# Optimization experiments

Measured on AMD Instinct MI355X. Metric: run time of the kernel, lower is better.

Reference implementation:

```python
import jax, jax.numpy as jnp
import numpy as np

N = 100_000   # nodes
E = 3_200_000 # edges
G = 128       # graphs in batch
H = 32        # hidden_dim
PI = float(np.pi)


def setup_inputs() -> dict:
    key = jax.random.key(0)
    ks = jax.random.split(key, 18)
    p = lambda k, s: (jax.random.normal(k, s, dtype=jnp.float32) * 0.1)
    x = jax.random.normal(ks[0], (N, 1), dtype=jnp.float32)
    edge_index = jax.random.randint(ks[1], (2, E), 0, N, dtype=jnp.int32)
    batch = jnp.sort(jax.random.randint(ks[2], (N,), 0, G, dtype=jnp.int32))
    return dict(
        x=x, edge_index=edge_index, batch=batch,
        W1=p(ks[3], (1, H)),  b1=jnp.zeros((H,), jnp.float32),
        W2=p(ks[4], (H, H)),  b2=jnp.zeros((H,), jnp.float32),
        W3=p(ks[5], (H, H)),  b3=jnp.zeros((H,), jnp.float32),
        Wt1=p(ks[6], (H, 32)), bt1=jnp.zeros((32,), jnp.float32),
        Wt2=p(ks[7], (32, 1)), bt2=jnp.zeros((1,), jnp.float32),
        Wg1=p(ks[8], (H, 32)), bg1=jnp.zeros((32,), jnp.float32),
        Wg2=p(ks[9], (32, 2)), bg2=jnp.zeros((2,), jnp.float32),
    )


def _gcn_norm(edge_index):
    # PyG GCNConv default: add self-loops, symmetric normalization.
    loop = jnp.arange(N, dtype=edge_index.dtype)
    src = jnp.concatenate([edge_index[0], loop])
    dst = jnp.concatenate([edge_index[1], loop])
    deg = jax.ops.segment_sum(jnp.ones_like(dst, dtype=jnp.float32), dst, num_segments=N)
    dinv = jnp.where(deg > 0, jax.lax.rsqrt(jnp.maximum(deg, 1.0)), 0.0)
    norm = dinv[src] * dinv[dst]  # [E+N]
    return src, dst, norm


def _gcn_conv(x, W, b, src, dst, norm):
    h = x @ W                                  # [N, out]
    msg = h[src] * norm[:, None]               # gather + scale  [E+N, out]
    return jax.ops.segment_sum(msg, dst, num_segments=N) + b


def _forward(x, W1, b1, W2, b2, W3, b3, Wt1, bt1, Wt2, bt2, Wg1, bg1, Wg2, bg2,
             edge_index, batch):
    src, dst, norm = _gcn_norm(edge_index)
    x = jax.nn.relu(_gcn_conv(x, W1, b1, src, dst, norm))
    x = jax.nn.relu(_gcn_conv(x, W2, b2, src, dst, norm))
    h = jax.nn.relu(_gcn_conv(x, W3, b3, src, dst, norm))
    # theta head per node
    theta = PI * jax.nn.sigmoid(jax.nn.relu(h @ Wt1 + bt1) @ Wt2 + bt2)[:, 0]  # [N]
    # global mean pool per graph
    counts = jax.ops.segment_sum(jnp.ones((N,), jnp.float32), batch, num_segments=G)
    gsum = jax.ops.segment_sum(h, batch, num_segments=G)
    gemb = gsum / jnp.maximum(counts, 1.0)[:, None]                            # [G, H]
    beta_gamma = 2.0 * PI * jax.nn.sigmoid(jax.nn.relu(gemb @ Wg1 + bg1) @ Wg2 + bg2)  # [G, 2]
    return theta, beta_gamma


def reference(x, edge_index, batch, W1, b1, W2, b2, W3, b3,
              Wt1, bt1, Wt2, bt2, Wg1, bg1, Wg2, bg2):
    return _forward(x, W1, b1, W2, b2, W3, b3, Wt1, bt1, Wt2, bt2,
                    Wg1, bg1, Wg2, bg2, edge_index, batch)
```

## Files before the change

kernel.cpp:

```cpp
#include <hip/hip_runtime.h>
#include <hip/hip_bf16.h>

#define PI_F 3.14159265358979323846f
#define NBLK 256
#define BSH 8
#define BSZ 256
#define SCAP 10240
#define SLDS 3072

static inline size_t align256(size_t x) { return (x + 255) & ~size_t(255); }

typedef float v2f __attribute__((ext_vector_type(2)));
typedef unsigned uvec4 __attribute__((ext_vector_type(4)));

__device__ __forceinline__ unsigned bfpack(float a, float b) {
    unsigned lo = (__float_as_uint(a) + 0x8000u) >> 16;
    unsigned hi = (__float_as_uint(b) + 0x8000u) & 0xFFFF0000u;
    return lo | hi;
}

__device__ __forceinline__ void f8acc(uint2 q, float rs, float acc[8]) {
    v2f l0 = __builtin_amdgcn_cvt_pk_f32_fp8(q.x, false);
    v2f h0 = __builtin_amdgcn_cvt_pk_f32_fp8(q.x, true);
    v2f l1 = __builtin_amdgcn_cvt_pk_f32_fp8(q.y, false);
    v2f h1 = __builtin_amdgcn_cvt_pk_f32_fp8(q.y, true);
    acc[0] += rs * l0.x; acc[1] += rs * l0.y; acc[2] += rs * h0.x; acc[3] += rs * h0.y;
    acc[4] += rs * l1.x; acc[5] += rs * l1.y; acc[6] += rs * h1.x; acc[7] += rs * h1.y;
}


__global__ void __launch_bounds__(1024) count_kernel(
                             const int* __restrict__ dst, int* __restrict__ C,
                             int E, int CHUNK, int NB2) {
    extern __shared__ int hist[];
    for (int i = threadIdx.x; i < NB2; i += 1024) hist[i] = 0;
    __syncthreads();
    int s0 = blockIdx.x * CHUNK, s1 = min(s0 + CHUNK, E);
    for (int e = s0 + threadIdx.x; e < s1; e += 1024)
        atomicAdd(&hist[dst[e] >> BSH], 1);
    __syncthreads();
    for (int i = threadIdx.x; i < NB2; i += 1024)
        C[(size_t)blockIdx.x * NB2 + i] = hist[i];
}

__global__ void scan_blocks_kernel(int* __restrict__ C, int* __restrict__ colsum, int NB2) {
    __shared__ int s[256];
    int k = blockIdx.x;
    int b = threadIdx.x;
    int v = C[(size_t)b * NB2 + k];
    s[b] = v;
    __syncthreads();
    for (int off = 1; off < 256; off <<= 1) {
        int w = (b >= off) ? s[b - off] : 0;
        __syncthreads();
        s[b] += w;
        __syncthreads();
    }
    C[(size_t)b * NB2 + k] = s[b] - v;
    if (b == 255) colsum[k] = s[255];
}

__global__ void scan_totals_kernel(const int* __restrict__ colsum, int* __restrict__ bbase,
                                   int NB2, int E) {
    __shared__ int s[256];
    __shared__ int running;
    if (threadIdx.x == 0) running = 0;
    __syncthreads();
    for (int base = 0; base < NB2; base += 256) {
        int i = base + threadIdx.x;
        int v = (i < NB2) ? colsum[i] : 0;
        s[threadIdx.x] = v;
        __syncthreads();
        for (int off = 1; off < 256; off <<= 1) {
            int w = (threadIdx.x >= (unsigned)off) ? s[threadIdx.x - off] : 0;
            __syncthreads();
            s[threadIdx.x] += w;
            __syncthreads();
        }
        if (i < NB2) bbase[i] = running + s[threadIdx.x] - v;
        __syncthreads();
        if (threadIdx.x == 255) running += s[255];
        __syncthreads();
    }
    if (threadIdx.x == 0) bbase[NB2] = E;
}

__global__ void __launch_bounds__(1024) scatter_kernel(
                               const int* __restrict__ src, const int* __restrict__ dst,
                               const int* __restrict__ C, const int* __restrict__ bbase,
                               unsigned* __restrict__ bkt_data, int E, int CHUNK, int NB2) {
    extern __shared__ int ofs[];
    for (int i = threadIdx.x; i < NB2; i += 1024)
        ofs[i] = bbase[i] + C[(size_t)blockIdx.x * NB2 + i];
    __syncthreads();
    int s0 = blockIdx.x * CHUNK, s1 = min(s0 + CHUNK, E);
    for (int e = s0 + threadIdx.x; e < s1; e += 1024) {
        int d = dst[e];
        int p = atomicAdd(&ofs[d >> BSH], 1);
        bkt_data[p] = ((unsigned)(d & (BSZ - 1)) << 17) | (unsigned)src[e];
    }
}

__global__ void __launch_bounds__(512) csr_build_kernel(
                                 const unsigned* __restrict__ bkt_data, const int* __restrict__ bbase,
                                 const float* __restrict__ x,
                                 unsigned* __restrict__ csr, int* __restrict__ e_start,
                                 float* __restrict__ dinv, float* __restrict__ xd,
                                 int N, int NB2) {
    __shared__ unsigned sdata[SCAP];
    __shared__ int hist[256];
    __shared__ int scn[256];
    __shared__ int bump[256];
    int tid = threadIdx.x;
    int b = blockIdx.x;
    int g0 = bbase[b], g1 = bbase[b + 1];
    int cnt = g1 - g0;
    bool fits = (cnt <= SCAP);
    if (tid < 256) hist[tid] = 0;
    __syncthreads();
    for (int i = tid; i < cnt; i += 512) {
        unsigned pk = bkt_data[g0 + i];
        if (fits) sdata[i] = pk;
        atomicAdd(&hist[pk >> 17], 1);
    }
    __syncthreads();
    int orig = (tid < 256) ? hist[tid] : 0;
    if (tid < 256) scn[tid] = orig;
    __syncthreads();
    for (int off = 1; off < 256; off <<= 1) {
        int w = (tid >= off && tid < 256) ? scn[tid - off] : 0;
        __syncthreads();
        if (tid < 256) scn[tid] += w;
        __syncthreads();
    }
    if (tid < 256) {
        int excl = scn[tid] - orig;
        bump[tid] = g0 + excl;
        int node = b * BSZ + tid;
        if (node < N) {
            float dv = rsqrtf((float)(orig + 1));
            dinv[node] = dv;
            xd[node] = x[node] * dv;
            e_start[node] = g0 + excl;
        }
    }
    if (b == NB2 - 1 && tid == 0) e_start[N] = g1;
    __syncthreads();
    for (int i = tid; i < cnt; i += 512) {
        unsigned pk = fits ? sdata[i] : bkt_data[g0 + i];
        int p = atomicAdd(&bump[pk >> 17], 1);
        csr[p] = pk & 0x1FFFFu;
    }
}


__device__ __forceinline__ void mm32_8(const float* __restrict__ sW, const float vr[8],
                                       int sub, int lane, float o[8]) {
    const float4* sW4 = (const float4*)sW;
    int base = lane & ~3;
#pragma unroll
    for (int r = 0; r < 4; r++) {
#pragma unroll
        for (int i = 0; i < 8; i++) {
            float vk = __shfl(vr[i], base | r, 64);
            int k = r * 8 + i;
            float4 w0 = sW4[k * 8 + sub * 2];
            float4 w1 = sW4[k * 8 + sub * 2 + 1];
            o[0] += vk * w0.x; o[1] += vk * w0.y; o[2] += vk * w0.z; o[3] += vk * w0.w;
            o[4] += vk * w1.x; o[5] += vk * w1.y; o[6] += vk * w1.z; o[7] += vk * w1.w;
        }
    }
}

__device__ __forceinline__ void store_f8(unsigned char* __restrict__ u8, float* __restrict__ uscale,
                                         int d, int sub, const float o[8]) {
    float am = 0.f;
#pragma unroll
    for (int i = 0; i < 8; i++) am = fmaxf(am, fabsf(o[i]));
    am = fmaxf(am, __shfl_xor(am, 1, 64));
    am = fmaxf(am, __shfl_xor(am, 2, 64));
    float rm = fmaxf(am, 1e-20f);
    float sc = 128.f / rm;
    unsigned w0 = 0, w1 = 0;
    w0 = __builtin_amdgcn_cvt_pk_fp8_f32(o[0] * sc, o[1] * sc, w0, false);
    w0 = __builtin_amdgcn_cvt_pk_fp8_f32(o[2] * sc, o[3] * sc, w0, true);
    w1 = __builtin_amdgcn_cvt_pk_fp8_f32(o[4] * sc, o[5] * sc, w1, false);
    w1 = __builtin_amdgcn_cvt_pk_fp8_f32(o[6] * sc, o[7] * sc, w1, true);
    uint2 st; st.x = w0; st.y = w1;
    ((uint2*)u8)[(size_t)d * 4 + sub] = st;
    if (sub == 0) uscale[d] = rm * (1.f / 128.f);
}

__device__ __forceinline__ bool stage_csr(const unsigned* __restrict__ csr,
                                          const int* __restrict__ e_start,
                                          int d0, int dEnd, int* sidx, int& E0) {
    E0 = e_start[d0];
    int E1 = e_start[dEnd];
    int m = E1 - E0;
    bool fits = (m <= SLDS);
    if (fits) {
        for (int i = threadIdx.x; i < m; i += 256)
            sidx[i] = (int)__builtin_nontemporal_load(&csr[E0 + i]);
    }
    __syncthreads();
    return fits;
}

__global__ void __launch_bounds__(256) agg1_kernel(
                            const float* __restrict__ xd, const int* __restrict__ e_start,
                            const unsigned* __restrict__ csr, const float* __restrict__ dinv,
                            const float* __restrict__ W1, const float* __restrict__ b1,
                            const float* __restrict__ W2,
                            unsigned char* __restrict__ u8o, float* __restrict__ uso, int n) {
    __shared__ float sW2[1024];
    __shared__ float sW1[32], sb1[32];
    __shared__ int sidx[SLDS];
    for (int i = threadIdx.x; i < 1024; i += 256) sW2[i] = W2[i];
    if (threadIdx.x < 32) { sW1[threadIdx.x] = W1[threadIdx.x]; sb1[threadIdx.x] = b1[threadIdx.x]; }
    int d0 = blockIdx.x * 64;
    int dEnd = min(d0 + 64, n);
    int E0;
    bool fits = stage_csr(csr, e_start, d0, dEnd, sidx, E0);
    int d = d0 + (threadIdx.x >> 2), sub = threadIdx.x & 3;
    int lane = threadIdx.x & 63;
    if (d >= n) return;
    int e0 = e_start[d];
    int cnt = e_start[d + 1] - e0;
    int l0 = e0 - E0;
    float s = 0.f;
    int j = sub;
    if (fits) {
        for (; j < cnt; j += 4) s += xd[sidx[l0 + j]];
    } else {
        for (; j < cnt; j += 4) s += xd[(int)csr[e0 + j]];
    }
    s += __shfl_xor(s, 1, 64);
    s += __shfl_xor(s, 2, 64);
    float dv = dinv[d];
    float tt = dv * (s + xd[d]);
    float vr[8];
#pragma unroll
    for (int i = 0; i < 8; i++) vr[i] = fmaxf(tt * sW1[sub * 8 + i] + sb1[sub * 8 + i], 0.f);
    float o[8];
#pragma unroll
    for (int i = 0; i < 8; i++) o[i] = 0.f;
    mm32_8(sW2, vr, sub, lane, o);
#pragma unroll
    for (int i = 0; i < 8; i++) o[i] *= dv;
    store_f8(u8o, uso, d, sub, o);
}

__device__ __forceinline__ void gather_f8(const unsigned char* __restrict__ u8,
                                          const float* __restrict__ uscale,
                                          const int* __restrict__ sidx, bool fits,
                                          const unsigned* __restrict__ csr,
                                          int e0, int l0, int cnt, int d, int sub, float acc[8]) {
#pragma unroll
    for (int i = 0; i < 8; i++) acc[i] = 0.f;
    const uint2* rows = (const uint2*)u8;
    int j = 0;
    if (fits) {
        for (; j + 8 <= cnt; j += 8) {
            int id[8];
#pragma unroll
            for (int k = 0; k < 8; k++) id[k] = sidx[l0 + j + k];
            float rs[8];
#pragma unroll
            for (int k = 0; k < 8; k++) rs[k] = uscale[id[k]];
            uint2 q[8];
#pragma unroll
            for (int k = 0; k < 8; k++) q[k] = rows[(size_t)id[k] * 4 + sub];
#pragma unroll
            for (int k = 0; k < 8; k++) f8acc(q[k], rs[k], acc);
        }
        for (; j < cnt; j++) {
            int i0 = sidx[l0 + j];
            f8acc(rows[(size_t)i0 * 4 + sub], uscale[i0], acc);
        }
    } else {
        for (; j + 4 <= cnt; j += 4) {
            int i0 = (int)csr[e0 + j],     i1 = (int)csr[e0 + j + 1];
            int i2 = (int)csr[e0 + j + 2], i3 = (int)csr[e0 + j + 3];
            float r0 = uscale[i0], r1 = uscale[i1], r2 = uscale[i2], r3 = uscale[i3];
            uint2 q0 = rows[(size_t)i0 * 4 + sub];
            uint2 q1 = rows[(size_t)i1 * 4 + sub];
            uint2 q2 = rows[(size_t)i2 * 4 + sub];
            uint2 q3 = rows[(size_t)i3 * 4 + sub];
            f8acc(q0, r0, acc); f8acc(q1, r1, acc); f8acc(q2, r2, acc); f8acc(q3, r3, acc);
        }
        for (; j < cnt; j++) {
            int i0 = (int)csr[e0 + j];
            f8acc(rows[(size_t)i0 * 4 + sub], uscale[i0], acc);
        }
    }
    f8acc(rows[(size_t)d * 4 + sub], uscale[d], acc);
}

__global__ void __launch_bounds__(256) agg2_kernel(
                            const unsigned char* __restrict__ u8, const float* __restrict__ uscale,
                            const int* __restrict__ e_start, const unsigned* __restrict__ csr,
                            const float* __restrict__ dinv, const float* __restrict__ bias,
                            const float* __restrict__ W,
                            unsigned char* __restrict__ o8, float* __restrict__ oscale, int n) {
    __shared__ float sW[1024];
    __shared__ float sb[32];
    __shared__ int sidx[SLDS];
    for (int i = threadIdx.x; i < 1024; i += 256) sW[i] = W[i];
    if (threadIdx.x < 32) sb[threadIdx.x] = bias[threadIdx.x];
    int d0 = blockIdx.x * 64;
    int dEnd = min(d0 + 64, n);
    int E0;
    bool fits = stage_csr(csr, e_start, d0, dEnd, sidx, E0);
    int d = d0 + (threadIdx.x >> 2), sub = threadIdx.x & 3;
    int lane = threadIdx.x & 63;
    if (d >= n) return;
    int e0 = e_start[d];
    int cnt = e_start[d + 1] - e0;
    float acc[8];
    gather_f8(u8, uscale, sidx, fits, csr, e0, e0 - E0, cnt, d, sub, acc);
    float dv = dinv[d];
    float vr[8];
#pragma unroll
    for (int i = 0; i < 8; i++) vr[i] = fmaxf(dv * acc[i] + sb[sub * 8 + i], 0.f);
    float o[8];
#pragma unroll
    for (int i = 0; i < 8; i++) o[i] = 0.f;
    mm32_8(sW, vr, sub, lane, o);
#pragma unroll
    for (int i = 0; i < 8; i++) o[i] *= dv;
    store_f8(o8, oscale, d, sub, o);
}

__global__ void __launch_bounds__(256) agg3_kernel(
                            const unsigned char* __restrict__ u8, const float* __restrict__ uscale,
                            const int* __restrict__ e_start, const unsigned* __restrict__ csr,
                            const float* __restrict__ dinv, const float* __restrict__ bias,
                            const float* __restrict__ Wt1, const float* __restrict__ bt1,
                            const float* __restrict__ Wt2, const float* __restrict__ bt2,
                            unsigned short* __restrict__ hb, float* __restrict__ theta, int n) {
    __shared__ float sW[1024];
    __shared__ float sb[32], sbt[32], sw2[32];
    __shared__ int sidx[SLDS];
    for (int i = threadIdx.x; i < 1024; i += 256) sW[i] = Wt1[i];
    if (threadIdx.x < 32) {
        sb[threadIdx.x] = bias[threadIdx.x];
        sbt[threadIdx.x] = bt1[threadIdx.x];
        sw2[threadIdx.x] = Wt2[threadIdx.x];
    }
    int d0 = blockIdx.x * 64;
    int dEnd = min(d0 + 64, n);
    int E0;
    bool fits = stage_csr(csr, e_start, d0, dEnd, sidx, E0);
    int d = d0 + (threadIdx.x >> 2), sub = threadIdx.x & 3;
    int lane = threadIdx.x & 63;
    if (d >= n) return;
    int e0 = e_start[d];
    int cnt = e_start[d + 1] - e0;
    float acc[8];
    gather_f8(u8, uscale, sidx, fits, csr, e0, e0 - E0, cnt, d, sub, acc);
    float dv = dinv[d];
    float vr[8];
#pragma unroll
    for (int i = 0; i < 8; i++) vr[i] = fmaxf(dv * acc[i] + sb[sub * 8 + i], 0.f);
    uvec4 st;
    st.x = bfpack(vr[0], vr[1]);
    st.y = bfpack(vr[2], vr[3]);
    st.z = bfpack(vr[4], vr[5]);
    st.w = bfpack(vr[6], vr[7]);
    __builtin_nontemporal_store(st, (uvec4*)hb + (size_t)d * 4 + sub);
    float o[8];
#pragma unroll
    for (int i = 0; i < 8; i++) o[i] = 0.f;
    mm32_8(sW, vr, sub, lane, o);
    float tl = 0.f;
#pragma unroll
    for (int i = 0; i < 8; i++)
        tl += fmaxf(o[i] + sbt[sub * 8 + i], 0.f) * sw2[sub * 8 + i];
    tl += __shfl_xor(tl, 1, 64);
    tl += __shfl_xor(tl, 2, 64);
    if (sub == 0) __builtin_nontemporal_store(PI_F / (1.f + __expf(-(tl + bt2[0]))), theta + d);
}


__global__ void gb_kernel(const int* __restrict__ batch, int* __restrict__ gstart,
                          int n, int G) {
    int i = blockIdx.x * 256 + threadIdx.x;
    if (i >= n) return;
    int g = batch[i];
    if (i == 0) {
        for (int gg = 0; gg <= g; gg++) gstart[gg] = 0;
    } else {
        int gp = batch[i - 1];
        for (int gg = gp + 1; gg <= g; gg++) gstart[gg] = i;
    }
    if (i == n - 1) {
        for (int gg = g + 1; gg <= G; gg++) gstart[gg] = n;
    }
}

__global__ void __launch_bounds__(512) bg_kernel(
                          const unsigned short* __restrict__ hb, const int* __restrict__ gstart,
                          const float* __restrict__ Wg1, const float* __restrict__ bg1v,
                          const float* __restrict__ Wg2, const float* __restrict__ bg2v,
                          float* __restrict__ out, int G) {
    __shared__ float sW[1024];
    __shared__ float part[8][32];
    for (int i = threadIdx.x; i < 1024; i += 512) sW[i] = Wg1[i];
    int g = blockIdx.x;
    int s = gstart[g], e = gstart[g + 1];
    int w = threadIdx.x >> 6;
    int lane = threadIdx.x & 63;
    int f = lane & 31, h = lane >> 5;
    float a = 0.f;
    for (int i = s + (w << 1) + h; i < e; i += 16)
        a += __uint_as_float((unsigned)hb[((size_t)i << 5) + f] << 16);
    a += __shfl_xor(a, 32, 64);
    if (h == 0) part[w][f] = a;
    __syncthreads();
    if (w == 0) {
        float hv = 0.f;
#pragma unroll
        for (int p = 0; p < 8; p++) hv += part[p][f];
        hv /= fmaxf((float)(e - s), 1.f);
        int base = lane & 32;
        float acc = bg1v[f];
#pragma unroll
        for (int k = 0; k < 32; k++) acc += __shfl(hv, base | k, 64) * sW[k * 32 + f];
        acc = fmaxf(acc, 0.f);
        float p0 = acc * Wg2[f * 2 + 0];
        float p1 = acc * Wg2[f * 2 + 1];
#pragma unroll
        for (int m = 1; m < 32; m <<= 1) {
            p0 += __shfl_xor(p0, m, 64);
            p1 += __shfl_xor(p1, m, 64);
        }
        if (lane == 0) {
            out[g * 2 + 0] = 2.f * PI_F / (1.f + __expf(-(p0 + bg2v[0])));
            out[g * 2 + 1] = 2.f * PI_F / (1.f + __expf(-(p1 + bg2v[1])));
        }
    }
}


extern "C" void kernel_launch(void* const* d_in, const int* in_sizes, int n_in,
                              void* d_out, int out_size, void* d_ws, size_t ws_size,
                              hipStream_t stream) {
    const float* x   = (const float*)d_in[0];
    const int*   ei  = (const int*)d_in[1];
    const int* batch = (const int*)d_in[2];
    const float* W1  = (const float*)d_in[3];
    const float* b1  = (const float*)d_in[4];
    const float* W2  = (const float*)d_in[5];
    const float* b2  = (const float*)d_in[6];
    const float* W3  = (const float*)d_in[7];
    const float* b3  = (const float*)d_in[8];
    const float* Wt1 = (const float*)d_in[9];
    const float* bt1 = (const float*)d_in[10];
    const float* Wt2 = (const float*)d_in[11];
    const float* bt2 = (const float*)d_in[12];
    const float* Wg1 = (const float*)d_in[13];
    const float* bg1 = (const float*)d_in[14];
    const float* Wg2 = (const float*)d_in[15];
    const float* bg2 = (const float*)d_in[16];

    const int N = in_sizes[0];
    const int E = in_sizes[1] / 2;
    const int G = 128;
    const int* src = ei;
    const int* dst = ei + E;
    float* theta_out = (float*)d_out;
    float* bg_out = (float*)d_out + N;

    const int NB2 = (N + BSZ - 1) >> BSH;
    const int CHUNK = (E + NBLK - 1) / NBLK;

    char* w = (char*)d_ws;
    auto alloc = [&](size_t bytes) -> char* { char* p = w; w += align256(bytes); return p; };
    int*      C        = (int*)alloc((size_t)NBLK * NB2 * 4);
    int*      colsum   = (int*)alloc((size_t)NB2 * 4);
    int*      bbase    = (int*)alloc((size_t)(NB2 + 1) * 4);
    unsigned* bkt_data = (unsigned*)alloc((size_t)E * 4);
    unsigned* csr      = (unsigned*)alloc((size_t)E * 4);
    int*      e_start  = (int*)alloc((size_t)(N + 1) * 4);
    float*    dinv     = (float*)alloc((size_t)N * 4);
    float*    xd       = (float*)alloc((size_t)N * 4);
    unsigned char* u2  = (unsigned char*)alloc((size_t)N * 32);
    float*    us2      = (float*)alloc((size_t)N * 4);
    unsigned char* u3  = (unsigned char*)alloc((size_t)N * 32);
    float*    us3      = (float*)alloc((size_t)N * 4);
    unsigned short* hb = (unsigned short*)alloc((size_t)N * 64);
    int*      gstart   = (int*)alloc((size_t)(G + 1) * 4);

    size_t ldsB = (size_t)NB2 * 4;
    count_kernel<<<NBLK, 1024, ldsB, stream>>>(dst, C, E, CHUNK, NB2);
    scan_blocks_kernel<<<NB2, 256, 0, stream>>>(C, colsum, NB2);
    scan_totals_kernel<<<1, 256, 0, stream>>>(colsum, bbase, NB2, E);
    scatter_kernel<<<NBLK, 1024, ldsB, stream>>>(src, dst, C, bbase, bkt_data, E, CHUNK, NB2);
    csr_build_kernel<<<NB2, 512, 0, stream>>>(bkt_data, bbase, x, csr, e_start, dinv, xd, N, NB2);
    gb_kernel<<<(N + 255) / 256, 256, 0, stream>>>(batch, gstart, N, G);

    unsigned gridQ = (unsigned)(((size_t)N * 4 + 255) / 256);

    agg1_kernel<<<gridQ, 256, 0, stream>>>(xd, e_start, csr, dinv, W1, b1, W2, u2, us2, N);
    agg2_kernel<<<gridQ, 256, 0, stream>>>(u2, us2, e_start, csr, dinv, b2, W3, u3, us3, N);
    agg3_kernel<<<gridQ, 256, 0, stream>>>(u3, us3, e_start, csr, dinv, b3,
                                           Wt1, bt1, Wt2, bt2, hb, theta_out, N);

    bg_kernel<<<G, 512, 0, stream>>>(hb, gstart, Wg1, bg1, Wg2, bg2, bg_out, G);
}
```

Baseline: 282.2 us.

## Split layer-2/3 gather across 8 threads per node with 16-byte row halves

The agg2 and agg3 kernels now assign 8 threads per destination node instead of 4. Each thread loads a 16-byte half-row of fp8 features for every fourth neighbor, and the partial sums are reduced with shuffles. The matmul is restructured to produce 16 outputs per thread, and the blocks shrink to 32 nodes with a smaller LDS index stage. The goal is more memory-level parallelism and wider loads in the latency-bound neighbor gather, at the cost of extra shuffle reductions, redundant matmul work across slots, and more blocks. The bg_kernel output guard also changes from lane==0 to f==0.

Result: no change. 287.6 us (+1.9%).

```diff
diff --git a/kernel.cpp b/kernel.cpp
--- a/kernel.cpp
+++ b/kernel.cpp
@@ -7,6 +7,7 @@
 #define BSZ 256
 #define SCAP 10240
 #define SLDS 3072
+#define SLDS3 1536
 
 static inline size_t align256(size_t x) { return (x + 255) & ~size_t(255); }
 
@@ -19,13 +20,14 @@
     return lo | hi;
 }
 
-__device__ __forceinline__ void f8acc(uint2 q, float rs, float acc[8]) {
-    v2f l0 = __builtin_amdgcn_cvt_pk_f32_fp8(q.x, false);
-    v2f h0 = __builtin_amdgcn_cvt_pk_f32_fp8(q.x, true);
-    v2f l1 = __builtin_amdgcn_cvt_pk_f32_fp8(q.y, false);
-    v2f h1 = __builtin_amdgcn_cvt_pk_f32_fp8(q.y, true);
-    acc[0] += rs * l0.x; acc[1] += rs * l0.y; acc[2] += rs * h0.x; acc[3] += rs * h0.y;
-    acc[4] += rs * l1.x; acc[5] += rs * l1.y; acc[6] += rs * h1.x; acc[7] += rs * h1.y;
+__device__ __forceinline__ void f8w(unsigned w, float rs, float* a) {
+    v2f lo = __builtin_amdgcn_cvt_pk_f32_fp8(w, false);
+    v2f hi = __builtin_amdgcn_cvt_pk_f32_fp8(w, true);
+    a[0] += rs * lo.x; a[1] += rs * lo.y; a[2] += rs * hi.x; a[3] += rs * hi.y;
+}
+
+__device__ __forceinline__ void f8acc16(uint4 q, float rs, float acc[16]) {
+    f8w(q.x, rs, acc); f8w(q.y, rs, acc + 4); f8w(q.z, rs, acc + 8); f8w(q.w, rs, acc + 12);
 }
 
 
@@ -154,6 +156,21 @@
 }
 
 
+__device__ __forceinline__ bool stage_csr(const unsigned* __restrict__ csr,
+                                          const int* __restrict__ e_start,
+                                          int d0, int dEnd, int* sidx, int cap, int& E0) {
+    E0 = e_start[d0];
+    int E1 = e_start[dEnd];
+    int m = E1 - E0;
+    bool fits = (m <= cap);
+    if (fits) {
+        for (int i = threadIdx.x; i < m; i += 256)
+            sidx[i] = (int)__builtin_nontemporal_load(&csr[E0 + i]);
+    }
+    __syncthreads();
+    return fits;
+}
+
 __device__ __forceinline__ void mm32_8(const float* __restrict__ sW, const float vr[8],
                                        int sub, int lane, float o[8]) {
     const float4* sW4 = (const float4*)sW;
@@ -172,8 +189,8 @@
     }
 }
 
-__device__ __forceinline__ void store_f8(unsigned char* __restrict__ u8, float* __restrict__ uscale,
-                                         int d, int sub, const float o[8]) {
+__device__ __forceinline__ void store_f8_q(unsigned char* __restrict__ u8, float* __restrict__ uscale,
+                                           int d, int sub, const float o[8]) {
     float am = 0.f;
 #pragma unroll
     for (int i = 0; i < 8; i++) am = fmaxf(am, fabsf(o[i]));
@@ -189,21 +206,6 @@
     uint2 st; st.x = w0; st.y = w1;
     ((uint2*)u8)[(size_t)d * 4 + sub] = st;
     if (sub == 0) uscale[d] = rm * (1.f / 128.f);
-}
-
-__device__ __forceinline__ bool stage_csr(const unsigned* __restrict__ csr,
-                                          const int* __restrict__ e_start,
-                                          int d0, int dEnd, int* sidx, int& E0) {
-    E0 = e_start[d0];
-    int E1 = e_start[dEnd];
-    int m = E1 - E0;
-    bool fits = (m <= SLDS);
-    if (fits) {
-        for (int i = threadIdx.x; i < m; i += 256)
-            sidx[i] = (int)__builtin_nontemporal_load(&csr[E0 + i]);
-    }
-    __syncthreads();
-    return fits;
 }
 
 __global__ void __launch_bounds__(256) agg1_kernel(
@@ -220,7 +222,7 @@
     int d0 = blockIdx.x * 64;
     int dEnd = min(d0 + 64, n);
     int E0;
-    bool fits = stage_csr(csr, e_start, d0, dEnd, sidx, E0);
+    bool fits = stage_csr(csr, e_start, d0, dEnd, sidx, SLDS, E0);
     int d = d0 + (threadIdx.x >> 2), sub = threadIdx.x & 3;
     int lane = threadIdx.x & 63;
     if (d >= n) return;
@@ -247,53 +249,75 @@
     mm32_8(sW2, vr, sub, lane, o);
 #pragma unroll
     for (int i = 0; i < 8; i++) o[i] *= dv;
-    store_f8(u8o, uso, d, sub, o);
-}
-
-__device__ __forceinline__ void gather_f8(const unsigned char* __restrict__ u8,
-                                          const float* __restrict__ uscale,
-                                          const int* __restrict__ sidx, bool fits,
-                                          const unsigned* __restrict__ csr,
-                                          int e0, int l0, int cnt, int d, int sub, float acc[8]) {
-#pragma unroll
-    for (int i = 0; i < 8; i++) acc[i] = 0.f;
-    const uint2* rows = (const uint2*)u8;
-    int j = 0;
+    store_f8_q(u8o, uso, d, sub, o);
+}
+
+
+__device__ __forceinline__ void gather_f8h(const unsigned char* __restrict__ u8,
+                                           const float* __restrict__ uscale,
+                                           const int* __restrict__ sidx, bool fits,
+                                           const unsigned* __restrict__ csr,
+                                           int e0, int l0, int cnt, int d,
+                                           int half, int slot, float acc[16]) {
+#pragma unroll
+    for (int i = 0; i < 16; i++) acc[i] = 0.f;
+    const uint4* rows = (const uint4*)u8;
+    int j = slot;
     if (fits) {
-        for (; j + 8 <= cnt; j += 8) {
-            int id[8];
-#pragma unroll
-            for (int k = 0; k < 8; k++) id[k] = sidx[l0 + j + k];
-            float rs[8];
-#pragma unroll
-            for (int k = 0; k < 8; k++) rs[k] = uscale[id[k]];
-            uint2 q[8];
-#pragma unroll
-            for (int k = 0; k < 8; k++) q[k] = rows[(size_t)id[k] * 4 + sub];
-#pragma unroll
-            for (int k = 0; k < 8; k++) f8acc(q[k], rs[k], acc);
-        }
-        for (; j < cnt; j++) {
-            int i0 = sidx[l0 + j];
-            f8acc(rows[(size_t)i0 * 4 + sub], uscale[i0], acc);
+        for (; j + 4 < cnt; j += 8) {
+            int ia = sidx[l0 + j];
+            int ib = sidx[l0 + j + 4];
+            float ra = uscale[ia], rb = uscale[ib];
+            uint4 qa = rows[(size_t)ia * 2 + half];
+            uint4 qb = rows[(size_t)ib * 2 + half];
+            f8acc16(qa, ra, acc);
+            f8acc16(qb, rb, acc);
+        }
+        if (j < cnt) {
+            int ia = sidx[l0 + j];
+            f8acc16(rows[(size_t)ia * 2 + half], uscale[ia], acc);
         }
     } else {
-        for (; j + 4 <= cnt; j += 4) {
-            int i0 = (int)csr[e0 + j],     i1 = (int)csr[e0 + j + 1];
-            int i2 = (int)csr[e0 + j + 2], i3 = (int)csr[e0 + j + 3];
-            float r0 = uscale[i0], r1 = uscale[i1], r2 = uscale[i2], r3 = uscale[i3];
-            uint2 q0 = rows[(size_t)i0 * 4 + sub];
-            uint2 q1 = rows[(size_t)i1 * 4 + sub];
-            uint2 q2 = rows[(size_t)i2 * 4 + sub];
-            uint2 q3 = rows[(size_t)i3 * 4 + sub];
-            f8acc(q0, r0, acc); f8acc(q1, r1, acc); f8acc(q2, r2, acc); f8acc(q3, r3, acc);
-        }
-        for (; j < cnt; j++) {
-            int i0 = (int)csr[e0 + j];
-            f8acc(rows[(size_t)i0 * 4 + sub], uscale[i0], acc);
-        }
-    }
-    f8acc(rows[(size_t)d * 4 + sub], uscale[d], acc);
+        for (; j + 4 < cnt; j += 8) {
+            int ia = (int)csr[e0 + j];
+            int ib = (int)csr[e0 + j + 4];
+            float ra = uscale[ia], rb = uscale[ib];
+            uint4 qa = rows[(size_t)ia * 2 + half];
+            uint4 qb = rows[(size_t)ib * 2 + half];
+            f8acc16(qa, ra, acc);
+            f8acc16(qb, rb, acc);
+        }
+        if (j < cnt) {
+            int ia = (int)csr[e0 + j];
+            f8acc16(rows[(size_t)ia * 2 + half], uscale[ia], acc);
+        }
+    }
+    if (slot == 0) {
+        f8acc16(rows[(size_t)d * 2 + half], uscale[d], acc);
+    }
+#pragma unroll
+    for (int i = 0; i < 16; i++) {
+        acc[i] += __shfl_xor(acc[i], 2, 64);
+        acc[i] += __shfl_xor(acc[i], 4, 64);
+    }
+}
+
+__device__ __forceinline__ void mm32_16(const float* __restrict__ sW, const float vr[16],
+                                        int half, int lane, float o[16]) {
+    const float4* sW4 = (const float4*)sW;
+    int nb = lane & ~7;
+#pragma unroll
+    for (int k = 0; k < 32; k++) {
+        float vk = __shfl(vr[k & 15], nb | (k >> 4), 64);
+        float4 w0 = sW4[k * 8 + half * 4 + 0];
+        float4 w1 = sW4[k * 8 + half * 4 + 1];
+        float4 w2 = sW4[k * 8 + half * 4 + 2];
+        float4 w3 = sW4[k * 8 + half * 4 + 3];
+        o[0]  += vk * w0.x; o[1]  += vk * w0.y; o[2]  += vk * w0.z; o[3]  += vk * w0.w;
+        o[4]  += vk * w1.x; o[5]  += vk * w1.y; o[6]  += vk * w1.z; o[7]  += vk * w1.w;
+        o[8]  += vk * w2.x; o[9]  += vk * w2.y; o[10] += vk * w2.z; o[11] += vk * w2.w;
+        o[12] += vk * w3.x; o[13] += vk * w3.y; o[14] += vk * w3.z; o[15] += vk * w3.w;
+    }
 }
 
 __global__ void __launch_bounds__(256) agg2_kernel(
@@ -304,31 +328,50 @@
                             unsigned char* __restrict__ o8, float* __restrict__ oscale, int n) {
     __shared__ float sW[1024];
     __shared__ float sb[32];
-    __shared__ int sidx[SLDS];
+    __shared__ int sidx[SLDS3];
     for (int i = threadIdx.x; i < 1024; i += 256) sW[i] = W[i];
     if (threadIdx.x < 32) sb[threadIdx.x] = bias[threadIdx.x];
-    int d0 = blockIdx.x * 64;
-    int dEnd = min(d0 + 64, n);
+    int d0 = blockIdx.x * 32;
+    int dEnd = min(d0 + 32, n);
     int E0;
-    bool fits = stage_csr(csr, e_start, d0, dEnd, sidx, E0);
-    int d = d0 + (threadIdx.x >> 2), sub = threadIdx.x & 3;
+    bool fits = stage_csr(csr, e_start, d0, dEnd, sidx, SLDS3, E0);
+    int d = d0 + (threadIdx.x >> 3);
+    int half = threadIdx.x & 1, slot = (threadIdx.x >> 1) & 3;
     int lane = threadIdx.x & 63;
     if (d >= n) return;
     int e0 = e_start[d];
     int cnt = e_start[d + 1] - e0;
-    float acc[8];
-    gather_f8(u8, uscale, sidx, fits, csr, e0, e0 - E0, cnt, d, sub, acc);
+    float acc[16];
+    gather_f8h(u8, uscale, sidx, fits, csr, e0, e0 - E0, cnt, d, half, slot, acc);
     float dv = dinv[d];
-    float vr[8];
-#pragma unroll
-    for (int i = 0; i < 8; i++) vr[i] = fmaxf(dv * acc[i] + sb[sub * 8 + i], 0.f);
-    float o[8];
-#pragma unroll
-    for (int i = 0; i < 8; i++) o[i] = 0.f;
-    mm32_8(sW, vr, sub, lane, o);
-#pragma unroll
-    for (int i = 0; i < 8; i++) o[i] *= dv;
-    store_f8(o8, oscale, d, sub, o);
+    float vr[16];
+#pragma unroll
+    for (int i = 0; i < 16; i++) vr[i] = fmaxf(dv * acc[i] + sb[half * 16 + i], 0.f);
+    float o[16];
+#pragma unroll
+    for (int i = 0; i < 16; i++) o[i] = 0.f;
+    mm32_16(sW, vr, half, lane, o);
+#pragma unroll
+    for (int i = 0; i < 16; i++) o[i] *= dv;
+    float am = 0.f;
+#pragma unroll
+    for (int i = 0; i < 16; i++) am = fmaxf(am, fabsf(o[i]));
+    am = fmaxf(am, __shfl_xor(am, 1, 64));
+    float rm = fmaxf(am, 1e-20f);
+    float sc = 128.f / rm;
+    unsigned w[4];
+#pragma unroll
+    for (int p = 0; p < 4; p++) {
+        unsigned t = 0;
+        t = __builtin_amdgcn_cvt_pk_fp8_f32(o[4 * p + 0] * sc, o[4 * p + 1] * sc, t, false);
+        t = __builtin_amdgcn_cvt_pk_fp8_f32(o[4 * p + 2] * sc, o[4 * p + 3] * sc, t, true);
+        w[p] = t;
+    }
+    if (slot == 0) {
+        uint4 st; st.x = w[0]; st.y = w[1]; st.z = w[2]; st.w = w[3];
+        ((uint4*)o8)[(size_t)d * 2 + half] = st;
+        if (half == 0) oscale[d] = rm * (1.f / 128.f);
+    }
 }
 
 __global__ void __launch_bounds__(256) agg3_kernel(
@@ -340,45 +383,49 @@
                             unsigned short* __restrict__ hb, float* __restrict__ theta, int n) {
     __shared__ float sW[1024];
     __shared__ float sb[32], sbt[32], sw2[32];
-    __shared__ int sidx[SLDS];
+    __shared__ int sidx[SLDS3];
     for (int i = threadIdx.x; i < 1024; i += 256) sW[i] = Wt1[i];
     if (threadIdx.x < 32) {
         sb[threadIdx.x] = bias[threadIdx.x];
         sbt[threadIdx.x] = bt1[threadIdx.x];
         sw2[threadIdx.x] = Wt2[threadIdx.x];
     }
-    int d0 = blockIdx.x * 64;
-    int dEnd = min(d0 + 64, n);
+    int d0 = blockIdx.x * 32;
+    int dEnd = min(d0 + 32, n);
     int E0;
-    bool fits = stage_csr(csr, e_start, d0, dEnd, sidx, E0);
-    int d = d0 + (threadIdx.x >> 2), sub = threadIdx.x & 3;
+    bool fits = stage_csr(csr, e_start, d0, dEnd, sidx, SLDS3, E0);
+    int d = d0 + (threadIdx.x >> 3);
+    int half = threadIdx.x & 1, slot = (threadIdx.x >> 1) & 3;
     int lane = threadIdx.x & 63;
     if (d >= n) return;
     int e0 = e_start[d];
     int cnt = e_start[d + 1] - e0;
-    float acc[8];
-    gather_f8(u8, uscale, sidx, fits, csr, e0, e0 - E0, cnt, d, sub, acc);
+    float acc[16];
+    gather_f8h(u8, uscale, sidx, fits, csr, e0, e0 - E0, cnt, d, half, slot, acc);
     float dv = dinv[d];
-    float vr[8];
-#pragma unroll
-    for (int i = 0; i < 8; i++) vr[i] = fmaxf(dv * acc[i] + sb[sub * 8 + i], 0.f);
-    uvec4 st;
-    st.x = bfpack(vr[0], vr[1]);
-    st.y = bfpack(vr[2], vr[3]);
-    st.z = bfpack(vr[4], vr[5]);
-    st.w = bfpack(vr[6], vr[7]);
-    __builtin_nontemporal_store(st, (uvec4*)hb + (size_t)d * 4 + sub);
-    float o[8];
-#pragma unroll
-    for (int i = 0; i < 8; i++) o[i] = 0.f;
-    mm32_8(sW, vr, sub, lane, o);
+    float vr[16];
+#pragma unroll
+    for (int i = 0; i < 16; i++) vr[i] = fmaxf(dv * acc[i] + sb[half * 16 + i], 0.f);
+    if (slot == 0) {
+        uvec4 s0, s1;
+        s0.x = bfpack(vr[0], vr[1]);   s0.y = bfpack(vr[2], vr[3]);
+        s0.z = bfpack(vr[4], vr[5]);   s0.w = bfpack(vr[6], vr[7]);
+        s1.x = bfpack(vr[8], vr[9]);   s1.y = bfpack(vr[10], vr[11]);
+        s1.z = bfpack(vr[12], vr[13]); s1.w = bfpack(vr[14], vr[15]);
+        __builtin_nontemporal_store(s0, (uvec4*)hb + (size_t)d * 4 + half * 2);
+        __builtin_nontemporal_store(s1, (uvec4*)hb + (size_t)d * 4 + half * 2 + 1);
+    }
+    float o[16];
+#pragma unroll
+    for (int i = 0; i < 16; i++) o[i] = 0.f;
+    mm32_16(sW, vr, half, lane, o);
     float tl = 0.f;
 #pragma unroll
-    for (int i = 0; i < 8; i++)
-        tl += fmaxf(o[i] + sbt[sub * 8 + i], 0.f) * sw2[sub * 8 + i];
+    for (int i = 0; i < 16; i++)
+        tl += fmaxf(o[i] + sbt[half * 16 + i], 0.f) * sw2[half * 16 + i];
     tl += __shfl_xor(tl, 1, 64);
-    tl += __shfl_xor(tl, 2, 64);
-    if (sub == 0) __builtin_nontemporal_store(PI_F / (1.f + __expf(-(tl + bt2[0]))), theta + d);
+    if (half == 0 && slot == 0)
+        __builtin_nontemporal_store(PI_F / (1.f + __expf(-(tl + bt2[0]))), theta + d);
 }
 
 
@@ -434,7 +481,7 @@
             p0 += __shfl_xor(p0, m, 64);
             p1 += __shfl_xor(p1, m, 64);
         }
-        if (lane == 0) {
+        if (f == 0) {
             out[g * 2 + 0] = 2.f * PI_F / (1.f + __expf(-(p0 + bg2v[0])));
             out[g * 2 + 1] = 2.f * PI_F / (1.f + __expf(-(p1 + bg2v[1])));
         }
@@ -500,10 +547,11 @@
     gb_kernel<<<(N + 255) / 256, 256, 0, stream>>>(batch, gstart, N, G);
 
     unsigned gridQ = (unsigned)(((size_t)N * 4 + 255) / 256);
+    unsigned gridH = (unsigned)(((size_t)N * 8 + 255) / 256);
 
     agg1_kernel<<<gridQ, 256, 0, stream>>>(xd, e_start, csr, dinv, W1, b1, W2, u2, us2, N);
-    agg2_kernel<<<gridQ, 256, 0, stream>>>(u2, us2, e_start, csr, dinv, b2, W3, u3, us3, N);
-    agg3_kernel<<<gridQ, 256, 0, stream>>>(u3, us3, e_start, csr, dinv, b3,
+    agg2_kernel<<<gridH, 256, 0, stream>>>(u2, us2, e_start, csr, dinv, b2, W3, u3, us3, N);
+    agg3_kernel<<<gridH, 256, 0, stream>>>(u3, us3, e_start, csr, dinv, b3,
                                            Wt1, bt1, Wt2, bt2, hb, theta_out, N);
 
     bg_kernel<<<G, 512, 0, stream>>>(hb, gstart, Wg1, bg1, Wg2, bg2, bg_out, G);
```
